# Optimization experiments

Hardware: AMD Instinct MI355X
Metric: run time of the kernel (lower is better)

## Reference

```python
import jax, jax.numpy as jnp
import numpy as np


def setup_inputs() -> dict:
    key = jax.random.key(0)
    ks = jax.random.split(key, 9)
    B, T, L, H2, E, V, OOV = 32, 48, 400, 512, 128, 50000, 100
    sd = lambda k, shape, s: jax.random.normal(k, shape, jnp.float32) * s
    return {
        "dec_hiddens": sd(ks[0], (B, T, H2), 1.0),   # decoder hidden state per step (B,T,2H)
        "enc_hiddens": sd(ks[1], (B, L, H2), 1.0),   # encoder outputs (B,L,2H)
        "W_enc": sd(ks[2], (H2, H2), 0.002),          # encoder-attention bilinear
        "W_dec": sd(ks[3], (H2, H2), 0.002),          # intra-decoder-attention bilinear
        "W_proj": sd(ks[4], (3 * H2, E), 0.02),       # decode2proj (6H -> emb)
        "W_vocab": sd(ks[5], (E, V), 0.05),           # proj2vocab (emb -> V, tied to embedding)
        "w_ptr": sd(ks[6], (3 * H2,), 0.02),          # ptr_gen weight
        "b_ptr": jnp.zeros((1,), jnp.float32),        # ptr_gen bias
        "extend_vocab": jax.random.randint(ks[7], (B, L), 0, V + OOV),
        "num_oov": OOV,
    }


def reference(dec_hiddens, enc_hiddens, W_enc, W_dec, W_proj, W_vocab,
              w_ptr, b_ptr, extend_vocab, num_oov):
    B, T, H2 = dec_hiddens.shape
    L = enc_hiddens.shape[1]
    V = W_vocab.shape[1]
    Vext = V + num_oov  # static python int
    rows = jnp.arange(B)[:, None]
    steps = jnp.arange(T)
    dec_seq = jnp.swapaxes(dec_hiddens, 0, 1)  # (T,B,2H) for scan

    def step(acc_exp, xs):
        h, t = xs  # h: (B,2H), t: scalar step index
        # intra-temporal encoder attention: exp(e) / running sum of previous exp(e)
        e = jnp.einsum('bh,hk,blk->bl', h, W_enc, enc_hiddens)  # (B,L)
        exp_e = jnp.exp(e)
        denom = jnp.where(t == 0, jnp.ones_like(acc_exp), acc_exp)
        temporal = exp_e / denom
        enc_att = temporal / temporal.sum(-1, keepdims=True)     # (B,L)
        enc_ctx = jnp.einsum('bl,blh->bh', enc_att, enc_hiddens)
        # intra-decoder attention over previous decoder hiddens (zeros at t=0)
        s = jnp.einsum('bh,hk,btk->bt', h, W_dec, dec_hiddens)   # (B,T)
        s = jnp.where((steps < t)[None, :], s, -1e30)
        datt = jax.nn.softmax(s, axis=-1)
        dec_ctx = jnp.where(t == 0, 0.0,
                            jnp.einsum('bt,bth->bh', datt, dec_hiddens))
        cat = jnp.concatenate([h, enc_ctx, dec_ctx], axis=-1)    # (B,6H)
        p = jax.nn.sigmoid(cat @ w_ptr + b_ptr)[:, None]         # (B,1) copy gate
        vocab_dist = jax.nn.softmax((cat @ W_proj) @ W_vocab, axis=-1)  # (B,V)
        # extended-vocab distribution: write softmax slice, scatter_add pointer dist
        final = jnp.zeros((B, Vext), dec_hiddens.dtype)
        final = final.at[:, :V].set((1.0 - p) * vocab_dist)
        final = final.at[rows, extend_vocab].add(p * enc_att)
        return acc_exp + exp_e, final

    init = jnp.zeros((B, L), dec_hiddens.dtype)
    _, out = jax.lax.scan(step, init, (dec_seq, steps))
    return jnp.swapaxes(out, 0, 1)  # (B,T,V+OOV)
```

## Files before the change

### kernel.cpp

```cpp
#include <hip/hip_runtime.h>
#include <hip/hip_bf16.h>
#include <cstdint>

typedef __attribute__((ext_vector_type(8))) short short8;
typedef __attribute__((ext_vector_type(4))) float floatx4;
typedef __attribute__((ext_vector_type(16))) float floatx16;

#define Bdim 32
#define Tdim 48
#define Ldim 400
#define Hdim 512
#define Edim 128
#define Vdim 50000
#define VEdim 50100
#define BTdim 1536
#define CATdim 1536
#define NPAD 50048
#define MTILES 96
#define NPART 782

__device__ __forceinline__ short f2bf(float x){
    __hip_bfloat16 h = __float2bfloat16(x);
    union { __hip_bfloat16 h; short s; } u; u.h = h; return u.s;
}

__device__ __forceinline__ float wred(float s){
    #pragma unroll
    for (int off = 32; off; off >>= 1) s += __shfl_xor(s, off, 64);
    return s;
}

template<bool BF16>
__device__ __forceinline__ void gemm_nn_body(
    const float* __restrict__ A, int lda,
    const float* __restrict__ B, int ldb,
    float* __restrict__ C, short* __restrict__ Cb, int ldc,
    int M, int N, int K, int m0, int n0,
    float (*As)[68], float (*Bs)[68])
{
    const int tid = threadIdx.x;
    const int tx = tid & 15, ty = tid >> 4;
    const int ar = tid >> 2, ac = (tid & 3) * 4;
    const int br = tid >> 4, bc = (tid & 15) * 4;
    float acc[4][4] = {};
    float4 va = make_float4(0.f,0.f,0.f,0.f);
    float4 vb = make_float4(0.f,0.f,0.f,0.f);
    if (m0 + ar < M) va = *(const float4*)(A + (size_t)(m0+ar)*lda + ac);
    if (n0 + bc < N) vb = *(const float4*)(B + (size_t)br*ldb + n0 + bc);
    for (int k0 = 0; k0 < K; k0 += 16){
        As[ac+0][ar]=va.x; As[ac+1][ar]=va.y; As[ac+2][ar]=va.z; As[ac+3][ar]=va.w;
        Bs[br][bc+0]=vb.x; Bs[br][bc+1]=vb.y; Bs[br][bc+2]=vb.z; Bs[br][bc+3]=vb.w;
        __syncthreads();
        const int kn = k0 + 16;
        if (kn < K){
            va = make_float4(0.f,0.f,0.f,0.f);
            vb = make_float4(0.f,0.f,0.f,0.f);
            if (m0 + ar < M) va = *(const float4*)(A + (size_t)(m0+ar)*lda + kn + ac);
            if (n0 + bc < N) vb = *(const float4*)(B + (size_t)(kn+br)*ldb + n0 + bc);
        }
        #pragma unroll
        for (int k=0;k<16;k++){
            float a[4], b[4];
            #pragma unroll
            for (int i=0;i<4;i++) a[i] = As[k][ty*4+i];
            #pragma unroll
            for (int j=0;j<4;j++) b[j] = Bs[k][tx*4+j];
            #pragma unroll
            for (int i=0;i<4;i++)
                #pragma unroll
                for (int j=0;j<4;j++)
                    acc[i][j] += a[i]*b[j];
        }
        __syncthreads();
    }
    #pragma unroll
    for (int i=0;i<4;i++){
        int m = m0 + ty*4 + i;
        if (m >= M) continue;
        #pragma unroll
        for (int j=0;j<4;j++){
            int n = n0 + tx*4 + j;
            if (n < N){
                if (BF16) Cb[(size_t)m*ldc + n] = f2bf(acc[i][j]);
                else      C[(size_t)m*ldc + n]  = acc[i][j];
            }
        }
    }
}

__device__ __forceinline__ void gemm_nt_body(
    const float* __restrict__ A, int lda,
    const float* __restrict__ B, int ldb,
    float* __restrict__ C, int ldc,
    int M, int N, int K, int m0, int n0,
    float (*As)[68], float (*Bs)[68])
{
    const int tid = threadIdx.x;
    const int tx = tid & 15, ty = tid >> 4;
    const int r = tid >> 2, c = (tid & 3) * 4;
    float acc[4][4] = {};
    float4 va = make_float4(0.f,0.f,0.f,0.f);
    float4 vb = make_float4(0.f,0.f,0.f,0.f);
    if (m0 + r < M) va = *(const float4*)(A + (size_t)(m0+r)*lda + c);
    if (n0 + r < N) vb = *(const float4*)(B + (size_t)(n0+r)*ldb + c);
    for (int k0 = 0; k0 < K; k0 += 16){
        As[c+0][r]=va.x; As[c+1][r]=va.y; As[c+2][r]=va.z; As[c+3][r]=va.w;
        Bs[c+0][r]=vb.x; Bs[c+1][r]=vb.y; Bs[c+2][r]=vb.z; Bs[c+3][r]=vb.w;
        __syncthreads();
        const int kn = k0 + 16;
        if (kn < K){
            va = make_float4(0.f,0.f,0.f,0.f);
            vb = make_float4(0.f,0.f,0.f,0.f);
            if (m0 + r < M) va = *(const float4*)(A + (size_t)(m0+r)*lda + kn + c);
            if (n0 + r < N) vb = *(const float4*)(B + (size_t)(n0+r)*ldb + kn + c);
        }
        #pragma unroll
        for (int k=0;k<16;k++){
            float a[4], b[4];
            #pragma unroll
            for (int i=0;i<4;i++) a[i] = As[k][ty*4+i];
            #pragma unroll
            for (int j=0;j<4;j++) b[j] = Bs[k][tx*4+j];
            #pragma unroll
            for (int i=0;i<4;i++)
                #pragma unroll
                for (int j=0;j<4;j++)
                    acc[i][j] += a[i]*b[j];
        }
        __syncthreads();
    }
    #pragma unroll
    for (int i=0;i<4;i++){
        int m = m0 + ty*4 + i;
        if (m >= M) continue;
        #pragma unroll
        for (int j=0;j<4;j++){
            int n = n0 + tx*4 + j;
            if (n < N) C[(size_t)m*ldc + n] = acc[i][j];
        }
    }
}

__global__ __launch_bounds__(256) void kA(
    const float* __restrict__ dec, const float* __restrict__ Wenc,
    const float* __restrict__ Wdec, float* __restrict__ P1, float* __restrict__ P2,
    float* __restrict__ cat,
    const float* __restrict__ Wv, short* __restrict__ Wt,
    const float* __restrict__ enc, const float* __restrict__ wptr,
    float* __restrict__ q_enc, float* __restrict__ q_dec,
    float* __restrict__ sums)
{
    __shared__ float As[16][68];
    __shared__ float Bs[16][68];
    int bid = blockIdx.x;
    if (bid < 384){
        int z = bid / 192, r = bid % 192;
        gemm_nn_body<false>(dec, Hdim, z ? Wdec : Wenc, Hdim,
                            z ? P2 : P1, nullptr, Hdim,
                            BTdim, Hdim, Hdim, (r>>3)*64, (r&7)*64, As, Bs);
        return;
    }
    bid -= 384;
    if (bid < 768){
        int idx = bid*256 + threadIdx.x;
        int m = idx >> 7, j = (idx & 127) << 2;
        *(float4*)(cat + (size_t)m*CATdim + j) =
            *(const float4*)(dec + (size_t)m*Hdim + j);
        return;
    }
    bid -= 768;
    if (bid < 6256){
        float (*tile)[33] = reinterpret_cast<float(*)[33]>(&As[0][0]);
        int n0 = (bid % 1564)*32, k0 = (bid / 1564)*32;
        int x = threadIdx.x & 31, y0 = threadIdx.x >> 5;
        for (int yy=y0; yy<32; yy+=8){
            int n = n0 + x;
            tile[yy][x] = (n < Vdim) ? Wv[(size_t)(k0+yy)*Vdim + n] : 0.f;
        }
        __syncthreads();
        for (int yy=y0; yy<32; yy+=8){
            int n = n0 + yy;
            if (n < NPAD) Wt[(size_t)n*Edim + k0 + x] = f2bf(tile[x][yy]);
        }
        return;
    }
    bid -= 6256;
    if (bid < 128){
        int b = bid >> 2, part = bid & 3;
        int wv = threadIdx.x >> 6, lane = threadIdx.x & 63;
        const float* w2 = wptr + Hdim;
        const float* w3 = wptr + 2*Hdim;
        for (int r = part*100 + wv; r < part*100 + 100; r += 4){
            const float* rp = enc + ((size_t)b*Ldim + r)*Hdim;
            float s = 0.f;
            #pragma unroll
            for (int i = 0; i < 8; i++) s += rp[lane + i*64]*w2[lane + i*64];
            s = wred(s);
            if (lane == 0) q_enc[b*Ldim + r] = s;
        }
        if (part == 0){
            for (int r = wv; r < Tdim; r += 4){
                const float* rp = dec + ((size_t)b*Tdim + r)*Hdim;
                float s = 0.f;
                #pragma unroll
                for (int i = 0; i < 8; i++) s += rp[lane + i*64]*w3[lane + i*64];
                s = wred(s);
                if (lane == 0) q_dec[b*Tdim + r] = s;
            }
        }
        return;
    }
    for (int i = threadIdx.x; i < BTdim; i += 256) sums[i] = 0.f;
}

__global__ __launch_bounds__(256) void kB(
    const float* __restrict__ P1, const float* __restrict__ P2,
    const float* __restrict__ enc, const float* __restrict__ dec,
    float* __restrict__ ebuf, float* __restrict__ sbuf)
{
    __shared__ float As[16][68];
    __shared__ float Bs[16][68];
    int bid = blockIdx.x;
    if (bid < 224){
        int z = bid / 7, x = bid % 7;
        gemm_nt_body(P1 + (size_t)z*Tdim*Hdim, Hdim,
                     enc + (size_t)z*Ldim*Hdim, Hdim,
                     ebuf + (size_t)z*Tdim*Ldim, Ldim,
                     Tdim, Ldim, Hdim, 0, x*64, As, Bs);
    } else {
        int z = bid - 224;
        gemm_nt_body(P2 + (size_t)z*Tdim*Hdim, Hdim,
                     dec + (size_t)z*Tdim*Hdim, Hdim,
                     sbuf + (size_t)z*Tdim*Tdim, Tdim,
                     Tdim, Tdim, Hdim, 0, 0, As, Bs);
    }
}

__global__ __launch_bounds__(512) void kC(
    const float* __restrict__ e, float* __restrict__ att, float* __restrict__ sbuf,
    const float* __restrict__ dec, const float* __restrict__ wptr,
    const float* __restrict__ bptr,
    const float* __restrict__ q_enc, const float* __restrict__ q_dec,
    float* __restrict__ pg)
{
    __shared__ float att_s[Tdim][Ldim];
    __shared__ float dE[Tdim], dD[Tdim], dH[Tdim];
    const int b = blockIdx.x;
    const int tid = threadIdx.x;
    if (tid < Ldim){
        const float* ep = e + (size_t)b*Tdim*Ldim + tid;
        float acc = 0.f;
        for (int t = 0; t < Tdim; ++t){
            float x = __expf(ep[t*Ldim]);
            att_s[t][tid] = x / (t ? acc : 1.f);
            acc += x;
        }
    }
    __syncthreads();
    const int wv = tid >> 6, lane = tid & 63;
    for (int t = wv; t < Tdim; t += 8){
        float s1 = 0.f, s2 = 0.f;
        for (int l = lane; l < Ldim; l += 64){
            float a = att_s[t][l];
            s1 += a;
            s2 += a * q_enc[b*Ldim + l];
        }
        s1 = wred(s1); s2 = wred(s2);
        float inv = 1.f/s1;
        if (lane == 0) dE[t] = s2*inv;
        for (int l = lane; l < Ldim; l += 64)
            att[(size_t)(b*Tdim + t)*Ldim + l] = att_s[t][l]*inv;
    }
    for (int t = wv; t < Tdim; t += 8){
        const float* hp = dec + ((size_t)b*Tdim + t)*Hdim;
        float s = 0.f;
        #pragma unroll
        for (int i = 0; i < 8; i++) s += hp[lane + i*64]*wptr[lane + i*64];
        s = wred(s);
        if (lane == 0) dH[t] = s;
    }
    for (int t = wv; t < Tdim; t += 8){
        float* row = sbuf + ((size_t)b*Tdim + t)*Tdim;
        if (t == 0){
            if (lane < Tdim) row[lane] = 0.f;
            if (lane == 0) dD[0] = 0.f;
        } else {
            float v = (lane < t) ? row[lane] : -1e30f;
            float mx = v;
            #pragma unroll
            for (int off = 32; off; off >>= 1) mx = fmaxf(mx, __shfl_xor(mx, off, 64));
            float ex = (lane < t) ? __expf(v - mx) : 0.f;
            float sm = wred(ex);
            float nv = ex / sm;
            if (lane < Tdim) row[lane] = nv;
            float d = (lane < Tdim) ? nv * q_dec[b*Tdim + lane] : 0.f;
            d = wred(d);
            if (lane == 0) dD[t] = d;
        }
    }
    __syncthreads();
    if (tid < Tdim){
        float tot = dH[tid] + dE[tid] + dD[tid] + bptr[0];
        pg[b*Tdim + tid] = 1.f/(1.f + __expf(-tot));
    }
}

__global__ __launch_bounds__(256) void kD(
    const float* __restrict__ att, const float* __restrict__ sbuf,
    const float* __restrict__ enc, const float* __restrict__ dec,
    float* __restrict__ cat)
{
    __shared__ float As[16][68];
    __shared__ float Bs[16][68];
    int bid = blockIdx.x;
    if (bid < 256){
        int z = bid >> 3, x = bid & 7;
        gemm_nn_body<false>(att + (size_t)z*Tdim*Ldim, Ldim,
                            enc + (size_t)z*Ldim*Hdim, Hdim,
                            cat + (size_t)z*Tdim*CATdim + Hdim, nullptr, CATdim,
                            Tdim, Hdim, Ldim, 0, x*64, As, Bs);
    } else {
        int r = bid - 256;
        int z = r >> 3, x = r & 7;
        gemm_nn_body<false>(sbuf + (size_t)z*Tdim*Tdim, Tdim,
                            dec + (size_t)z*Tdim*Hdim, Hdim,
                            cat + (size_t)z*Tdim*CATdim + 2*Hdim, nullptr, CATdim,
                            Tdim, Hdim, Tdim, 0, x*64, As, Bs);
    }
}

__global__ __launch_bounds__(256) void kE(
    const float* __restrict__ cat, const float* __restrict__ Wproj,
    short* __restrict__ projb)
{
    __shared__ float As[16][68];
    __shared__ float Bs[16][68];
    int by = blockIdx.x >> 1, bx = blockIdx.x & 1;
    gemm_nn_body<true>(cat, CATdim, Wproj, Edim,
                       nullptr, projb, Edim,
                       BTdim, Edim, CATdim, by*64, bx*64, As, Bs);
}

__global__ __launch_bounds__(256) void kF(
    const short* __restrict__ Ab, const short* __restrict__ Bt,
    float* __restrict__ sums)
{
    const int lane = threadIdx.x & 63;
    const int wave = threadIdx.x >> 6;
    const int l15 = lane & 15, quad = lane >> 4;
    const int wid = blockIdx.x*4 + wave;
    if (wid >= NPART) return;
    const int n0 = wid*64;
    short8 bfrag[4][4];
    #pragma unroll
    for (int ct=0;ct<4;ct++){
        const short* bp = Bt + (size_t)(n0 + ct*16 + l15)*Edim + quad*8;
        #pragma unroll
        for (int kk=0;kk<4;kk++) bfrag[ct][kk] = *(const short8*)(bp + kk*32);
    }
    float vmask[4];
    #pragma unroll
    for (int ct=0;ct<4;ct++) vmask[ct] = (n0 + ct*16 < Vdim) ? 1.f : 0.f;

    auto loadA = [&](int mt, short8 (&af)[4]){
        const short* ap = Ab + (size_t)(mt*16 + l15)*Edim + quad*8;
        #pragma unroll
        for (int kk=0;kk<4;kk++) af[kk] = *(const short8*)(ap + kk*32);
    };
    auto compute = [&](int mt, short8 (&af)[4]){
        floatx4 a0 = {0.f,0.f,0.f,0.f};
        floatx4 a1 = a0, a2 = a0, a3 = a0;
        #pragma unroll
        for (int kk=0;kk<4;kk++){
            a0 = __builtin_amdgcn_mfma_f32_16x16x32_bf16(bfrag[0][kk], af[kk], a0, 0, 0, 0);
            a1 = __builtin_amdgcn_mfma_f32_16x16x32_bf16(bfrag[1][kk], af[kk], a1, 0, 0, 0);
            a2 = __builtin_amdgcn_mfma_f32_16x16x32_bf16(bfrag[2][kk], af[kk], a2, 0, 0, 0);
            a3 = __builtin_amdgcn_mfma_f32_16x16x32_bf16(bfrag[3][kk], af[kk], a3, 0, 0, 0);
        }
        float s = vmask[0]*(__expf(a0[0])+__expf(a0[1])+__expf(a0[2])+__expf(a0[3]))
                + vmask[1]*(__expf(a1[0])+__expf(a1[1])+__expf(a1[2])+__expf(a1[3]))
                + vmask[2]*(__expf(a2[0])+__expf(a2[1])+__expf(a2[2])+__expf(a2[3]))
                + vmask[3]*(__expf(a3[0])+__expf(a3[1])+__expf(a3[2])+__expf(a3[3]));
        s += __shfl_xor(s, 16, 64);
        s += __shfl_xor(s, 32, 64);
        if (lane < 16)
            atomicAdd(&sums[mt*16 + l15], s);
    };

    const int mt0 = blockIdx.y*48, mt1 = mt0 + 48;
    short8 afA[4], afB[4];
    loadA(mt0, afA);
    for (int mt=mt0; mt<mt1; mt+=2){
        loadA(mt+1, afB);
        compute(mt, afA);
        if (mt+2 < mt1) loadA(mt+2, afA);
        compute(mt+1, afB);
    }
}

__global__ __launch_bounds__(256) void kG(
    const short* __restrict__ Ab, const short* __restrict__ Bt,
    const float* __restrict__ sums, const float* __restrict__ pg,
    const float* __restrict__ att, const int* __restrict__ ev,
    float* __restrict__ out)
{
    __shared__ float scl[768];
    __shared__ int hits[6400];
    __shared__ int hcnt;
    const int lane = threadIdx.x & 63;
    const int wave = threadIdx.x >> 6;
    const int l31 = lane & 31, half = lane >> 5;
    const int n0 = blockIdx.x*128 + wave*32;
    const int n = n0 + l31;
    const int yoff = blockIdx.y*768;
    const int mt0 = blockIdx.y*24;
    for (int i = threadIdx.x; i < 768; i += 256){
        int m = yoff + i;
        scl[i] = (1.f - pg[m]) / sums[m];
    }
    if (threadIdx.x == 0) hcnt = 0;
    __syncthreads();

    if (n0 >= Vdim){
        if (n < VEdim){
            for (int mt=mt0; mt<mt0+24; ++mt){
                #pragma unroll
                for (int r=0;r<16;r++){
                    int m = mt*32 + (r&3) + 8*(r>>2) + 4*half;
                    out[(size_t)m*VEdim + n] = 0.f;
                }
            }
        }
    } else {
        short8 bfrag[8];
        const short* bp = Bt + (size_t)n*Edim + half*8;
        #pragma unroll
        for (int kk=0;kk<8;kk++) bfrag[kk] = *(const short8*)(bp + kk*16);
        const bool valid = n < Vdim;
        for (int mt=mt0; mt<mt0+24; ++mt){
            floatx16 acc;
            #pragma unroll
            for (int i=0;i<16;i++) acc[i] = 0.f;
            const short* ap = Ab + (size_t)(mt*32 + l31)*Edim + half*8;
            #pragma unroll
            for (int kk=0;kk<8;kk++){
                short8 af = *(const short8*)(ap + kk*16);
                acc = __builtin_amdgcn_mfma_f32_32x32x16_bf16(af, bfrag[kk], acc, 0, 0, 0);
            }
            #pragma unroll
            for (int r=0;r<16;r++){
                int m = mt*32 + (r&3) + 8*(r>>2) + 4*half;
                if (valid) out[(size_t)m*VEdim + n] = scl[m - yoff]*__expf(acc[r]);
                else if (n < VEdim) out[(size_t)m*VEdim + n] = 0.f;
            }
        }
    }
    for (int idx = threadIdx.x; idx < 16*Ldim; idx += 256){
        int b = (blockIdx.y << 4) + idx/Ldim;
        int l = idx % Ldim;
        int v = ev[b*Ldim + l];
        if ((v >> 7) == (int)blockIdx.x){
            int h = atomicAdd(&hcnt, 1);
            hits[h] = (v << 14) | ((b & 31) << 9) | l;
        }
    }
    __syncthreads();
    const int tot = hcnt * Tdim;
    for (int j = threadIdx.x; j < tot; j += 256){
        int h = j / Tdim, t = j % Tdim;
        int pk = hits[h];
        int v = pk >> 14;
        int b = (pk >> 9) & 31;
        int l = pk & 511;
        int m = b*Tdim + t;
        atomicAdd(&out[(size_t)m*VEdim + v], pg[m]*att[(size_t)m*Ldim + l]);
    }
}

extern "C" void kernel_launch(void* const* d_in, const int* in_sizes, int n_in,
                              void* d_out, int out_size, void* d_ws, size_t ws_size,
                              hipStream_t stream)
{
    const float* dec  = (const float*)d_in[0];
    const float* enc  = (const float*)d_in[1];
    const float* Wenc = (const float*)d_in[2];
    const float* Wdec = (const float*)d_in[3];
    const float* Wproj= (const float*)d_in[4];
    const float* Wvoc = (const float*)d_in[5];
    const float* wptr = (const float*)d_in[6];
    const float* bptr = (const float*)d_in[7];
    const int*   ev   = (const int*)d_in[8];
    float* out = (float*)d_out;

    float* ws = (float*)d_ws;
    float* P1    = ws;
    float* P2    = P1 + 786432;
    float* ebuf  = P2 + 786432;
    float* att   = ebuf + 614400;
    float* sbuf  = att + 614400;
    float* cat   = sbuf + 73728;
    float* q_enc = cat + 2359296;
    float* q_dec = q_enc + 12800;
    float* pg    = q_dec + 1536;
    float* sums  = pg + 1536;
    short* projb = (short*)(sums + 1536);
    short* Wt    = projb + 196608;

    dim3 blk(256);
    kA<<<dim3(7537), blk, 0, stream>>>(dec, Wenc, Wdec, P1, P2, cat,
                                       Wvoc, Wt, enc, wptr, q_enc, q_dec, sums);
    kB<<<dim3(256), blk, 0, stream>>>(P1, P2, enc, dec, ebuf, sbuf);
    kC<<<dim3(Bdim), dim3(512), 0, stream>>>(ebuf, att, sbuf, dec, wptr, bptr,
                                             q_enc, q_dec, pg);
    kD<<<dim3(512), blk, 0, stream>>>(att, sbuf, enc, dec, cat);
    kE<<<dim3(48), blk, 0, stream>>>(cat, Wproj, projb);
    kF<<<dim3(196,2), blk, 0, stream>>>(projb, Wt, sums);
    kG<<<dim3(392,2), blk, 0, stream>>>(projb, Wt, sums, pg, att, ev, out);
}
```

Before: 746.9 us.

## Store concat activations in bf16, use MFMA for projection, replace atomics with partial-sum reduction

The concatenated decoder/context activations are now written as bf16 by kA and kD. The W_proj matrix is transposed to bf16 in kA so that kE can run a 32x32x16 bf16 MFMA GEMM instead of the fp32 shared-memory tiled GEMM. kF no longer accumulates softmax denominators with atomicAdd; it writes per-wave partial sums to a buffer, and a new kRed kernel reduces them and precomputes the per-row scale used by kG. This removes atomic contention and the slow fp32 projection, at the cost of an extra kernel launch, a larger partials buffer, and the loss of the 2-way y-split in kF.

New measurement: 696.5 us. -6.8%, faster.

```diff
diff --git a/kernel.cpp b/kernel.cpp
--- a/kernel.cpp
+++ b/kernel.cpp
@@ -18,6 +18,7 @@
 #define NPAD 50048
 #define MTILES 96
 #define NPART 782
+#define NPSTRIDE 800
 
 __device__ __forceinline__ short f2bf(float x){
     __hip_bfloat16 h = __float2bfloat16(x);
@@ -144,11 +145,11 @@
 __global__ __launch_bounds__(256) void kA(
     const float* __restrict__ dec, const float* __restrict__ Wenc,
     const float* __restrict__ Wdec, float* __restrict__ P1, float* __restrict__ P2,
-    float* __restrict__ cat,
+    short* __restrict__ catb,
     const float* __restrict__ Wv, short* __restrict__ Wt,
+    const float* __restrict__ Wproj, short* __restrict__ WpT,
     const float* __restrict__ enc, const float* __restrict__ wptr,
-    float* __restrict__ q_enc, float* __restrict__ q_dec,
-    float* __restrict__ sums)
+    float* __restrict__ q_enc, float* __restrict__ q_dec)
 {
     __shared__ float As[16][68];
     __shared__ float Bs[16][68];
@@ -161,14 +162,18 @@
         return;
     }
     bid -= 384;
-    if (bid < 768){
+    if (bid < 384){
         int idx = bid*256 + threadIdx.x;
-        int m = idx >> 7, j = (idx & 127) << 2;
-        *(float4*)(cat + (size_t)m*CATdim + j) =
-            *(const float4*)(dec + (size_t)m*Hdim + j);
+        int m = idx >> 6, j = (idx & 63) << 3;
+        float4 v0 = *(const float4*)(dec + (size_t)m*Hdim + j);
+        float4 v1 = *(const float4*)(dec + (size_t)m*Hdim + j + 4);
+        short8 s;
+        s[0]=f2bf(v0.x); s[1]=f2bf(v0.y); s[2]=f2bf(v0.z); s[3]=f2bf(v0.w);
+        s[4]=f2bf(v1.x); s[5]=f2bf(v1.y); s[6]=f2bf(v1.z); s[7]=f2bf(v1.w);
+        *(short8*)(catb + (size_t)m*CATdim + j) = s;
         return;
     }
-    bid -= 768;
+    bid -= 384;
     if (bid < 6256){
         float (*tile)[33] = reinterpret_cast<float(*)[33]>(&As[0][0]);
         int n0 = (bid % 1564)*32, k0 = (bid / 1564)*32;
@@ -185,7 +190,19 @@
         return;
     }
     bid -= 6256;
-    if (bid < 128){
+    if (bid < 192){
+        float (*tile)[33] = reinterpret_cast<float(*)[33]>(&As[0][0]);
+        int k0 = (bid / 4)*32, n0 = (bid % 4)*32;
+        int x = threadIdx.x & 31, y0 = threadIdx.x >> 5;
+        for (int yy=y0; yy<32; yy+=8)
+            tile[yy][x] = Wproj[(size_t)(k0+yy)*Edim + n0 + x];
+        __syncthreads();
+        for (int yy=y0; yy<32; yy+=8)
+            WpT[(size_t)(n0+yy)*CATdim + k0 + x] = f2bf(tile[x][yy]);
+        return;
+    }
+    bid -= 192;
+    {
         int b = bid >> 2, part = bid & 3;
         int wv = threadIdx.x >> 6, lane = threadIdx.x & 63;
         const float* w2 = wptr + Hdim;
@@ -208,9 +225,7 @@
                 if (lane == 0) q_dec[b*Tdim + r] = s;
             }
         }
-        return;
-    }
-    for (int i = threadIdx.x; i < BTdim; i += 256) sums[i] = 0.f;
+    }
 }
 
 __global__ __launch_bounds__(256) void kB(
@@ -308,42 +323,57 @@
 __global__ __launch_bounds__(256) void kD(
     const float* __restrict__ att, const float* __restrict__ sbuf,
     const float* __restrict__ enc, const float* __restrict__ dec,
-    float* __restrict__ cat)
+    short* __restrict__ catb)
 {
     __shared__ float As[16][68];
     __shared__ float Bs[16][68];
     int bid = blockIdx.x;
     if (bid < 256){
         int z = bid >> 3, x = bid & 7;
-        gemm_nn_body<false>(att + (size_t)z*Tdim*Ldim, Ldim,
-                            enc + (size_t)z*Ldim*Hdim, Hdim,
-                            cat + (size_t)z*Tdim*CATdim + Hdim, nullptr, CATdim,
-                            Tdim, Hdim, Ldim, 0, x*64, As, Bs);
+        gemm_nn_body<true>(att + (size_t)z*Tdim*Ldim, Ldim,
+                           enc + (size_t)z*Ldim*Hdim, Hdim,
+                           nullptr, catb + (size_t)z*Tdim*CATdim + Hdim, CATdim,
+                           Tdim, Hdim, Ldim, 0, x*64, As, Bs);
     } else {
         int r = bid - 256;
         int z = r >> 3, x = r & 7;
-        gemm_nn_body<false>(sbuf + (size_t)z*Tdim*Tdim, Tdim,
-                            dec + (size_t)z*Tdim*Hdim, Hdim,
-                            cat + (size_t)z*Tdim*CATdim + 2*Hdim, nullptr, CATdim,
-                            Tdim, Hdim, Tdim, 0, x*64, As, Bs);
+        gemm_nn_body<true>(sbuf + (size_t)z*Tdim*Tdim, Tdim,
+                           dec + (size_t)z*Tdim*Hdim, Hdim,
+                           nullptr, catb + (size_t)z*Tdim*CATdim + 2*Hdim, CATdim,
+                           Tdim, Hdim, Tdim, 0, x*64, As, Bs);
     }
 }
 
 __global__ __launch_bounds__(256) void kE(
-    const float* __restrict__ cat, const float* __restrict__ Wproj,
+    const short* __restrict__ catb, const short* __restrict__ WpT,
     short* __restrict__ projb)
 {
-    __shared__ float As[16][68];
-    __shared__ float Bs[16][68];
-    int by = blockIdx.x >> 1, bx = blockIdx.x & 1;
-    gemm_nn_body<true>(cat, CATdim, Wproj, Edim,
-                       nullptr, projb, Edim,
-                       BTdim, Edim, CATdim, by*64, bx*64, As, Bs);
+    const int lane = threadIdx.x & 63;
+    const int wave = threadIdx.x >> 6;
+    const int l31 = lane & 31, half = lane >> 5;
+    const int mt = blockIdx.x;
+    const int n0 = wave*32;
+    const short* ap = catb + (size_t)(mt*32 + l31)*CATdim + half*8;
+    const short* bp = WpT  + (size_t)(n0 + l31)*CATdim + half*8;
+    floatx16 acc;
+    #pragma unroll
+    for (int i=0;i<16;i++) acc[i] = 0.f;
+    #pragma unroll 4
+    for (int kk=0;kk<96;kk++){
+        short8 af = *(const short8*)(ap + kk*16);
+        short8 bf = *(const short8*)(bp + kk*16);
+        acc = __builtin_amdgcn_mfma_f32_32x32x16_bf16(af, bf, acc, 0, 0, 0);
+    }
+    #pragma unroll
+    for (int r=0;r<16;r++){
+        int m = mt*32 + (r&3) + 8*(r>>2) + 4*half;
+        projb[(size_t)m*Edim + n0 + l31] = f2bf(acc[r]);
+    }
 }
 
 __global__ __launch_bounds__(256) void kF(
     const short* __restrict__ Ab, const short* __restrict__ Bt,
-    float* __restrict__ sums)
+    float* __restrict__ partial)
 {
     const int lane = threadIdx.x & 63;
     const int wave = threadIdx.x >> 6;
@@ -384,23 +414,37 @@
         s += __shfl_xor(s, 16, 64);
         s += __shfl_xor(s, 32, 64);
         if (lane < 16)
-            atomicAdd(&sums[mt*16 + l15], s);
+            partial[(size_t)(mt*16 + l15)*NPSTRIDE + wid] = s;
     };
 
-    const int mt0 = blockIdx.y*48, mt1 = mt0 + 48;
     short8 afA[4], afB[4];
-    loadA(mt0, afA);
-    for (int mt=mt0; mt<mt1; mt+=2){
+    loadA(0, afA);
+    for (int mt=0; mt<MTILES; mt+=2){
         loadA(mt+1, afB);
         compute(mt, afA);
-        if (mt+2 < mt1) loadA(mt+2, afA);
+        if (mt+2 < MTILES) loadA(mt+2, afA);
         compute(mt+1, afB);
     }
+}
+
+__global__ __launch_bounds__(256) void kRed(const float* __restrict__ partial,
+                         const float* __restrict__ pg, float* __restrict__ scale){
+    int m = blockIdx.x;
+    float s = 0.f;
+    for (int w = threadIdx.x; w < NPART; w += 256)
+        s += partial[(size_t)m*NPSTRIDE + w];
+    #pragma unroll
+    for (int off=32; off; off>>=1) s += __shfl_down(s, off, 64);
+    __shared__ float red[4];
+    if ((threadIdx.x&63)==0) red[threadIdx.x>>6]=s;
+    __syncthreads();
+    if (threadIdx.x==0)
+        scale[m] = (1.f - pg[m]) / (red[0]+red[1]+red[2]+red[3]);
 }
 
 __global__ __launch_bounds__(256) void kG(
     const short* __restrict__ Ab, const short* __restrict__ Bt,
-    const float* __restrict__ sums, const float* __restrict__ pg,
+    const float* __restrict__ scale, const float* __restrict__ pg,
     const float* __restrict__ att, const int* __restrict__ ev,
     float* __restrict__ out)
 {
@@ -414,10 +458,8 @@
     const int n = n0 + l31;
     const int yoff = blockIdx.y*768;
     const int mt0 = blockIdx.y*24;
-    for (int i = threadIdx.x; i < 768; i += 256){
-        int m = yoff + i;
-        scl[i] = (1.f - pg[m]) / sums[m];
-    }
+    for (int i = threadIdx.x; i < 768; i += 256)
+        scl[i] = scale[yoff + i];
     if (threadIdx.x == 0) hcnt = 0;
     __syncthreads();
 
@@ -498,22 +540,26 @@
     float* ebuf  = P2 + 786432;
     float* att   = ebuf + 614400;
     float* sbuf  = att + 614400;
-    float* cat   = sbuf + 73728;
-    float* q_enc = cat + 2359296;
+    float* q_enc = sbuf + 73728;
     float* q_dec = q_enc + 12800;
     float* pg    = q_dec + 1536;
-    float* sums  = pg + 1536;
-    short* projb = (short*)(sums + 1536);
-    short* Wt    = projb + 196608;
+    float* scale = pg + 1536;
+    float* partial = scale + 1536;
+    short* catb  = (short*)(partial + (size_t)BTdim*NPSTRIDE);
+    short* projb = catb + (size_t)BTdim*CATdim;
+    short* WpT   = projb + 196608;
+    short* Wt    = WpT + 196608;
 
     dim3 blk(256);
-    kA<<<dim3(7537), blk, 0, stream>>>(dec, Wenc, Wdec, P1, P2, cat,
-                                       Wvoc, Wt, enc, wptr, q_enc, q_dec, sums);
+    kA<<<dim3(7344), blk, 0, stream>>>(dec, Wenc, Wdec, P1, P2, catb,
+                                       Wvoc, Wt, Wproj, WpT, enc, wptr,
+                                       q_enc, q_dec);
     kB<<<dim3(256), blk, 0, stream>>>(P1, P2, enc, dec, ebuf, sbuf);
     kC<<<dim3(Bdim), dim3(512), 0, stream>>>(ebuf, att, sbuf, dec, wptr, bptr,
                                              q_enc, q_dec, pg);
-    kD<<<dim3(512), blk, 0, stream>>>(att, sbuf, enc, dec, cat);
-    kE<<<dim3(48), blk, 0, stream>>>(cat, Wproj, projb);
-    kF<<<dim3(196,2), blk, 0, stream>>>(projb, Wt, sums);
-    kG<<<dim3(392,2), blk, 0, stream>>>(projb, Wt, sums, pg, att, ev, out);
-}
+    kD<<<dim3(512), blk, 0, stream>>>(att, sbuf, enc, dec, catb);
+    kE<<<dim3(48), blk, 0, stream>>>(catb, WpT, projb);
+    kF<<<dim3(196), blk, 0, stream>>>(projb, Wt, partial);
+    kRed<<<dim3(BTdim), blk, 0, stream>>>(partial, pg, scale);
+    kG<<<dim3(392,2), blk, 0, stream>>>(projb, Wt, scale, pg, att, ev, out);
+}
```
